# Kernel optimization log

Hardware: AMD Instinct MI355X
Metric: run time of the kernel (lower is better)

Reference implementation:

```python
import jax, jax.numpy as jnp
import numpy as np

EMB = 1024
HEADS = 16
EPS = 1e-6


def setup_inputs() -> dict:
    key = jax.random.key(0)
    ks = jax.random.split(key, 11)
    B, T = 4, 2048
    s = 0.02
    inp = {
        "x": jax.random.normal(ks[0], (B, T, EMB), dtype=jnp.float32),
        "Wq": jax.random.normal(ks[1], (EMB, EMB), dtype=jnp.float32) * s,
        "bq": jnp.zeros((EMB,), dtype=jnp.float32),
        "Wk": jax.random.normal(ks[2], (EMB, EMB), dtype=jnp.float32) * s,
        "bk": jnp.zeros((EMB,), dtype=jnp.float32),
        "Wv": jax.random.normal(ks[3], (EMB, EMB), dtype=jnp.float32) * s,
        "bv": jnp.zeros((EMB,), dtype=jnp.float32),
        "Wp": jax.random.normal(ks[4], (EMB, EMB), dtype=jnp.float32) * s,
        "bp": jnp.zeros((EMB,), dtype=jnp.float32),
        "gamma": jnp.ones((EMB,), dtype=jnp.float32),
        "beta": jnp.zeros((EMB,), dtype=jnp.float32),
    }
    return inp


def reference(x, Wq, bq, Wk, bk, Wv, bv, Wp, bp, gamma, beta):
    B, T, E = x.shape
    H = HEADS
    hd = E // H
    residual = x
    # torch Linear: y = x @ W.T + b
    q = (jnp.einsum('bte,fe->btf', x, Wq) + bq).reshape(B, T, H, hd).transpose(0, 2, 1, 3)
    k = (jnp.einsum('bte,fe->btf', x, Wk) + bk).reshape(B, T, H, hd).transpose(0, 2, 1, 3)
    v = (jnp.einsum('bte,fe->btf', x, Wv) + bv).reshape(B, T, H, hd).transpose(0, 2, 1, 3)
    # NOTE: original scales by 1/sqrt(T), not 1/sqrt(head_size)
    scale = 1.0 / jnp.sqrt(jnp.asarray(T, dtype=x.dtype))
    att = jnp.einsum('bhqd,bhkd->bhqk', q, k) * scale
    causal = jnp.tril(jnp.ones((T, T), dtype=bool))
    att = jnp.where(causal, att, -jnp.inf)
    att = jax.nn.softmax(att, axis=-1)
    out = jnp.einsum('bhqk,bhkd->bhqd', att, v)
    out = out.transpose(0, 2, 1, 3).reshape(B, T, E)
    # residual added BEFORE projection (as in original)
    out = jnp.einsum('bte,fe->btf', out + residual, Wp) + bp
    # LayerNorm(eps=1e-6)
    mu = jnp.mean(out, axis=-1, keepdims=True)
    var = jnp.mean(jnp.square(out - mu), axis=-1, keepdims=True)
    out = (out - mu) / jnp.sqrt(var + EPS) * gamma + beta
    return out
```

## Files before the change

### kernel.cpp

```cpp
#include <hip/hip_runtime.h>
#include <hip/hip_bf16.h>
#include <cstdint>
#include <cstdio>

#define EMB    1024
#define HEADS  16
#define HD     64
#define TSEQ   2048
#define NBATCH 4
#define BT     (NBATCH*TSEQ)
#define QKVN   3072
#define QKLD   2048

#define CSCALE (1.4426950408889634f * 0.022097086912079608f)

typedef __hip_bfloat16 bf16;
typedef __attribute__((ext_vector_type(8))) short short8;
typedef __attribute__((ext_vector_type(4))) short short4v;
typedef __attribute__((ext_vector_type(4))) float f32x4;

#define MFMA32(A,B,C) __builtin_amdgcn_mfma_f32_16x16x32_bf16(A,B,C,0,0,0)
#if __has_builtin(__builtin_amdgcn_mfma_f32_16x16x16_bf16)
#define MFMA16(A,B,C) __builtin_amdgcn_mfma_f32_16x16x16_bf16(A,B,C,0,0,0)
#else
#define MFMA16(A,B,C) __builtin_amdgcn_mfma_f32_16x16x16bf16_1k(A,B,C,0,0,0)
#endif

#if __has_builtin(__builtin_amdgcn_exp2f)
#define EXP2(x) __builtin_amdgcn_exp2f(x)
#else
#define EXP2(x) exp2f(x)
#endif

template<bool B> struct BoolC { static constexpr bool value = B; };

__device__ __forceinline__ void gload_lds16(const void* g, void* l) {
  __builtin_amdgcn_global_load_lds(
      (const __attribute__((address_space(1))) void*)g,
      (__attribute__((address_space(3))) void*)l,
      16, 0, 0);
}

__device__ __forceinline__ unsigned pkbf(float a, float b) {
  unsigned ua = __builtin_bit_cast(unsigned, a) + 0x8000u;
  unsigned ub = __builtin_bit_cast(unsigned, b) + 0x8000u;
  return __builtin_amdgcn_perm(ub, ua, 0x07060302u);
}

__global__ void fused_cast(const float* __restrict__ x, const float* __restrict__ Wq,
                           const float* __restrict__ Wk, const float* __restrict__ Wv,
                           const float* __restrict__ Wp, const float* __restrict__ bq,
                           const float* __restrict__ bk, const float* __restrict__ bv,
                           bf16* __restrict__ xb, bf16* __restrict__ wqkv,
                           bf16* __restrict__ wpb, float* __restrict__ biasqkv) {
  const int blk = blockIdx.x;
  const int i = threadIdx.x * 4;
  if (blk >= 12288) {
    const int wsel = blk - 12288;
    const float* bsrc = wsel == 0 ? bq : (wsel == 1 ? bk : bv);
    float4 bv4 = *(const float4*)(bsrc + i);
    if (wsel == 0) { bv4.x *= CSCALE; bv4.y *= CSCALE; bv4.z *= CSCALE; bv4.w *= CSCALE; }
    *(float4*)(biasqkv + wsel * 1024 + i) = bv4;
    return;
  }
  const float* src; bf16* dst; float sc = 1.0f;
  if (blk < 8192)       { src = x  + (size_t)blk * 1024;           dst = xb   + (size_t)blk * 1024; }
  else if (blk < 9216)  { src = Wq + (size_t)(blk - 8192) * 1024;  dst = wqkv + (size_t)(blk - 8192) * 1024; sc = CSCALE; }
  else if (blk < 10240) { src = Wk + (size_t)(blk - 9216) * 1024;  dst = wqkv + ((size_t)1 << 20) + (size_t)(blk - 9216) * 1024; }
  else if (blk < 11264) { src = Wv + (size_t)(blk - 10240) * 1024; dst = wqkv + ((size_t)2 << 20) + (size_t)(blk - 10240) * 1024; }
  else                  { src = Wp + (size_t)(blk - 11264) * 1024; dst = wpb  + (size_t)(blk - 11264) * 1024; }
  float4 v = *(const float4*)(src + i);
  union { short4v v; bf16 b[4]; } u;
  u.b[0] = __float2bfloat16(v.x * sc); u.b[1] = __float2bfloat16(v.y * sc);
  u.b[2] = __float2bfloat16(v.z * sc); u.b[3] = __float2bfloat16(v.w * sc);
  *(short4v*)(dst + i) = u.v;
}

template<int MODE>
__global__ __launch_bounds__(256) void gemm_bt(
    const bf16* __restrict__ A, const bf16* __restrict__ B,
    const float* __restrict__ bias, void* __restrict__ out0,
    bf16* __restrict__ vt, int M, int N, int K) {
  __shared__ bf16 As[128 * 32];
  __shared__ bf16 Bs[128 * 32];
  const int tid = threadIdx.x;
  const int l = tid & 63, w = tid >> 6;
  const int r = l & 15, q = l >> 4;
  const int m0 = blockIdx.y * 128, n0 = blockIdx.x * 128;
  const int wm = w >> 1, wn = w & 1;

  f32x4 acc[4][4];
#pragma unroll
  for (int i = 0; i < 4; ++i)
#pragma unroll
    for (int j = 0; j < 4; ++j) acc[i][j] = (f32x4){0.f, 0.f, 0.f, 0.f};

  const int slot0 = w * 64 + l;
  const int rowS0 = slot0 >> 2, chS0 = (slot0 & 3) * 8;
  const int slot1 = 256 + slot0;
  const int rowS1 = slot1 >> 2, chS1 = (slot1 & 3) * 8;

  const bf16* A0 = A + (size_t)(m0 + rowS0) * K + chS0;
  const bf16* A1 = A + (size_t)(m0 + rowS1) * K + chS1;
  const bf16* B0 = B + (size_t)(n0 + rowS0) * K + chS0;
  const bf16* B1 = B + (size_t)(n0 + rowS1) * K + chS1;
  char* AsD0 = (char*)As + w * 1024;
  char* AsD1 = (char*)As + 4096 + w * 1024;
  char* BsD0 = (char*)Bs + w * 1024;
  char* BsD1 = (char*)Bs + 4096 + w * 1024;

  for (int k0 = 0; k0 < K; k0 += 32) {
    __syncthreads();
    gload_lds16(A0 + k0, AsD0);
    gload_lds16(A1 + k0, AsD1);
    gload_lds16(B0 + k0, BsD0);
    gload_lds16(B1 + k0, BsD1);
    __syncthreads();

    short8 af[4], bfr[4];
#pragma unroll
    for (int mt = 0; mt < 4; ++mt)
      af[mt] = *(const short8*)(As + (wm * 64 + mt * 16 + r) * 32 + q * 8);
#pragma unroll
    for (int nt = 0; nt < 4; ++nt)
      bfr[nt] = *(const short8*)(Bs + (wn * 64 + nt * 16 + r) * 32 + q * 8);
#pragma unroll
    for (int mt = 0; mt < 4; ++mt)
#pragma unroll
      for (int nt = 0; nt < 4; ++nt)
        acc[mt][nt] = MFMA32(af[mt], bfr[nt], acc[mt][nt]);
  }

#pragma unroll
  for (int nt = 0; nt < 4; ++nt) {
    const int col = n0 + wn * 64 + nt * 16 + r;
    const float bv = bias[col];
#pragma unroll
    for (int mt = 0; mt < 4; ++mt) {
#pragma unroll
      for (int reg = 0; reg < 4; ++reg) {
        const int row = m0 + wm * 64 + mt * 16 + q * 4 + reg;
        const float v = acc[mt][nt][reg] + bv;
        if (MODE == 1) {
          ((float*)out0)[(size_t)row * N + col] = v;
        } else if (n0 < 2048) {
          ((bf16*)out0)[(size_t)row * QKLD + col] = __float2bfloat16(v);
        } else {
          const int f = col - 2048, h = f >> 6, d = f & 63;
          const int b = row >> 11, t = row & 2047;
          const int swz = (t & ~63) | ((((t >> 3) ^ d) & 7) << 3) | (t & 7);
          vt[((size_t)(b * 16 + h) * 64 + d) * 2048 + swz] = __float2bfloat16(v);
        }
      }
    }
  }
}

__global__ __launch_bounds__(256, 2) void flash5(
    const bf16* __restrict__ qk, const bf16* __restrict__ vt,
    const float* __restrict__ x, bf16* __restrict__ pb) {
  const int bh = blockIdx.x;
  const int ip = blockIdx.y;
  const int b = bh >> 4, h = bh & 15;
  const int qt[4] = { 31 - ip, 23 - ip, ip + 8, ip };
  const int tid = threadIdx.x, l = tid & 63, w = tid >> 6;
  const int r = l & 15, quad = l >> 4;

  __shared__ bf16 VtL[2][64 * 64];

  const bf16* Qbase = qk + (size_t)b * TSEQ * QKLD + h * HD;
  const bf16* Kbase = Qbase + 1024;
  const bf16* Vhead = vt + (size_t)bh * 64 * 2048;

  const int sl0 = tid, sl1 = 256 + tid;
  const bf16* vg0 = Vhead + (size_t)(sl0 >> 3) * 2048 + (sl0 & 7) * 8;
  const bf16* vg1 = Vhead + (size_t)(sl1 >> 3) * 2048 + (sl1 & 7) * 8;
  char* ldsb0[2] = { (char*)&VtL[0][0] + w * 1024, (char*)&VtL[1][0] + w * 1024 };
  char* ldsb1[2] = { (char*)&VtL[0][0] + 4096 + w * 1024, (char*)&VtL[1][0] + 4096 + w * 1024 };

  short8 qf0[4], qf1[4];
#pragma unroll
  for (int t = 0; t < 4; ++t) {
    const bf16* qp = Qbase + (size_t)(qt[t] * 64 + w * 16 + r) * QKLD + quad * 8;
    qf0[t] = *(const short8*)qp;
    qf1[t] = *(const short8*)(qp + 32);
  }

  f32x4 o[4][4], lac[4];
#pragma unroll
  for (int t = 0; t < 4; ++t) {
    lac[t] = (f32x4){0.f, 0.f, 0.f, 0.f};
#pragma unroll
    for (int nt = 0; nt < 4; ++nt) o[t][nt] = (f32x4){0.f, 0.f, 0.f, 0.f};
  }

  short4v ones4;
#pragma unroll
  for (int j = 0; j < 4; ++j) ones4[j] = (short)0x3F80;

  short8 kf0[4], kf1[4];
  short4v vf[4][4];

  gload_lds16(vg0, ldsb0[0]);
  gload_lds16(vg1, ldsb1[0]);
  int bsel = 0;

  const int ktmax = qt[0];
  const int qrow_l = w * 16 + r;
  for (int kt = 0; kt <= ktmax; ++kt) {
#pragma unroll
    for (int g = 0; g < 4; ++g) {
      const bf16* kp = Kbase + (size_t)(kt * 64 + g * 16 + r) * QKLD + quad * 8;
      kf0[g] = *(const short8*)kp;
      kf1[g] = *(const short8*)(kp + 32);
    }
    __syncthreads();
    if (kt < ktmax) {
      gload_lds16(vg0 + (kt + 1) * 64, ldsb0[bsel ^ 1]);
      gload_lds16(vg1 + (kt + 1) * 64, ldsb1[bsel ^ 1]);
    }
    {
      const bf16* V = &VtL[bsel][0];
#pragma unroll
      for (int nt = 0; nt < 4; ++nt)
#pragma unroll
        for (int g = 0; g < 4; ++g)
          vf[nt][g] = *(const short4v*)(V + (nt * 16 + r) * 64 +
                                        (((g * 2 + (quad >> 1)) ^ (r & 7)) * 8) + (quad & 1) * 4);
    }

    auto tilestep = [&](int t, auto diagc) {
      constexpr bool D = decltype(diagc)::value;
      f32x4 s[4];
#pragma unroll
      for (int g = 0; g < 4; ++g) {
        f32x4 a = (f32x4){0.f, 0.f, 0.f, 0.f};
        a = MFMA32(kf0[g], qf0[t], a);
        a = MFMA32(kf1[g], qf1[t], a);
        s[g] = a;
      }
      short4v pA[4];
#pragma unroll
      for (int g = 0; g < 4; ++g) {
        float p[4];
#pragma unroll
        for (int reg = 0; reg < 4; ++reg) {
          float e = EXP2(s[g][reg]);
          if (D) {
            const int kj = g * 16 + quad * 4 + reg;
            if (kj > qrow_l) e = 0.f;
          }
          p[reg] = e;
        }
        union { short4v v; unsigned u[2]; } pu;
        pu.u[0] = pkbf(p[0], p[1]);
        pu.u[1] = pkbf(p[2], p[3]);
        pA[g] = pu.v;
      }
#pragma unroll
      for (int nt = 0; nt < 4; ++nt)
#pragma unroll
        for (int g = 0; g < 4; ++g)
          o[t][nt] = MFMA16(pA[g], vf[nt][g], o[t][nt]);
#pragma unroll
      for (int g = 0; g < 4; ++g)
        lac[t] = MFMA16(pA[g], ones4, lac[t]);
    };

    if (kt == qt[0]) tilestep(0, BoolC<true>{}); else tilestep(0, BoolC<false>{});
    if (kt <= qt[1]) { if (kt == qt[1]) tilestep(1, BoolC<true>{}); else tilestep(1, BoolC<false>{}); }
    if (kt <= qt[2]) { if (kt == qt[2]) tilestep(2, BoolC<true>{}); else tilestep(2, BoolC<false>{}); }
    if (kt <= qt[3]) { if (kt == qt[3]) tilestep(3, BoolC<true>{}); else tilestep(3, BoolC<false>{}); }
    bsel ^= 1;
  }

#pragma unroll
  for (int t = 0; t < 4; ++t) {
#pragma unroll
    for (int reg = 0; reg < 4; ++reg) {
      const float inv = 1.0f / lac[t][reg];
      const int row = qt[t] * 64 + w * 16 + quad * 4 + reg;
      const float* xr = x + (size_t)(b * TSEQ + row) * EMB + h * HD;
      bf16* pr = pb + (size_t)(b * TSEQ + row) * EMB + h * HD;
#pragma unroll
      for (int nt = 0; nt < 4; ++nt) {
        const int d = nt * 16 + r;
        pr[d] = __float2bfloat16(o[t][nt][reg] * inv + xr[d]);
      }
    }
  }
}

__global__ __launch_bounds__(256) void ln_kernel(float* __restrict__ out,
                                                 const float* __restrict__ gamma,
                                                 const float* __restrict__ beta) {
  const int row = blockIdx.x;
  const int tid = threadIdx.x;
  float* p = out + (size_t)row * EMB;
  float4 v = ((const float4*)p)[tid];
  float s = v.x + v.y + v.z + v.w;
  float ss = v.x * v.x + v.y * v.y + v.z * v.z + v.w * v.w;
#pragma unroll
  for (int m = 1; m < 64; m <<= 1) {
    s += __shfl_xor(s, m, 64);
    ss += __shfl_xor(ss, m, 64);
  }
  __shared__ float red[8];
  const int w = tid >> 6, l = tid & 63;
  if (l == 0) { red[w] = s; red[4 + w] = ss; }
  __syncthreads();
  s = red[0] + red[1] + red[2] + red[3];
  ss = red[4] + red[5] + red[6] + red[7];
  const float mu = s * (1.0f / EMB);
  const float var = ss * (1.0f / EMB) - mu * mu;
  const float rs = rsqrtf(var + 1e-6f);
  const float4 g = ((const float4*)gamma)[tid];
  const float4 bb = ((const float4*)beta)[tid];
  float4 o;
  o.x = (v.x - mu) * rs * g.x + bb.x;
  o.y = (v.y - mu) * rs * g.y + bb.y;
  o.z = (v.z - mu) * rs * g.z + bb.z;
  o.w = (v.w - mu) * rs * g.w + bb.w;
  ((float4*)p)[tid] = o;
}

extern "C" void kernel_launch(void* const* d_in, const int* in_sizes, int n_in,
                              void* d_out, int out_size, void* d_ws, size_t ws_size,
                              hipStream_t stream) {
  const float* x     = (const float*)d_in[0];
  const float* Wq    = (const float*)d_in[1];
  const float* bq    = (const float*)d_in[2];
  const float* Wk    = (const float*)d_in[3];
  const float* bk    = (const float*)d_in[4];
  const float* Wv    = (const float*)d_in[5];
  const float* bv    = (const float*)d_in[6];
  const float* Wp    = (const float*)d_in[7];
  const float* bp    = (const float*)d_in[8];
  const float* gamma = (const float*)d_in[9];
  const float* beta  = (const float*)d_in[10];
  float* out = (float*)d_out;

  if (ws_size < (size_t)74 * 1024 * 1024) {
    printf("kernel_launch: ws_size %zu too small\n", ws_size);
    return;
  }
  char* ws = (char*)d_ws;
  bf16* xb    = (bf16*)ws;
  bf16* wqkv  = (bf16*)(ws + ((size_t)16 << 20));
  bf16* wpb   = (bf16*)(ws + ((size_t)22 << 20));
  float* bqkv = (float*)(ws + ((size_t)24 << 20));
  bf16* qkbuf = (bf16*)(ws + ((size_t)25 << 20));
  bf16* vtbuf = (bf16*)(ws + ((size_t)57 << 20));
  bf16* pbuf  = xb;

  fused_cast<<<12291, 256, 0, stream>>>(x, Wq, Wk, Wv, Wp, bq, bk, bv, xb, wqkv, wpb, bqkv);

  gemm_bt<0><<<dim3(24, 64), 256, 0, stream>>>(xb, wqkv, bqkv, qkbuf, vtbuf, BT, QKVN, EMB);

  flash5<<<dim3(64, 8), 256, 0, stream>>>(qkbuf, vtbuf, x, pbuf);

  gemm_bt<1><<<dim3(8, 64), 256, 0, stream>>>(pbuf, wpb, bp, out, nullptr, BT, EMB, EMB);

  ln_kernel<<<BT, 256, 0, stream>>>(out, gamma, beta);
}
```

Measured before the change: 311.7 us.

## Replace QKV GEMM with 256x256 double-buffered 8-wave pipelined kernel

Adds a new QKV projection GEMM that uses 256x256 output tiles, 512 threads, a 64-wide K step and double-buffered LDS. Global-to-LDS loads are interleaved with four MFMA phases per tile, using explicit barriers, vmcnt waits and s_setprio. It also applies an XOR-swizzled LDS layout and a grouped block-to-tile mapping aimed at L2 reuse. The goal is to hide memory latency and raise MFMA utilisation compared with the 128x128 generic kernel. In exchange it relies on hand-tuned wait counts, and the large accumulator arrays add register pressure.

```diff
diff --git a/kernel.cpp b/kernel.cpp
--- a/kernel.cpp
+++ b/kernel.cpp
@@ -46,6 +46,13 @@
   unsigned ub = __builtin_bit_cast(unsigned, b) + 0x8000u;
   return __builtin_amdgcn_perm(ub, ua, 0x07060302u);
 }
+
+#define BARRIER() do { asm volatile("" ::: "memory"); \
+                       __builtin_amdgcn_s_barrier(); \
+                       asm volatile("" ::: "memory"); } while (0)
+#define BAR_VM(N) do { asm volatile("s_waitcnt vmcnt(" #N ")" ::: "memory"); \
+                       __builtin_amdgcn_s_barrier(); \
+                       asm volatile("" ::: "memory"); } while (0)
 
 __global__ void fused_cast(const float* __restrict__ x, const float* __restrict__ Wq,
                            const float* __restrict__ Wk, const float* __restrict__ Wv,
@@ -74,6 +81,150 @@
   u.b[0] = __float2bfloat16(v.x * sc); u.b[1] = __float2bfloat16(v.y * sc);
   u.b[2] = __float2bfloat16(v.z * sc); u.b[3] = __float2bfloat16(v.w * sc);
   *(short4v*)(dst + i) = u.v;
+}
+
+#define PHASE_MFMA(MI0, NJ0) do { \
+  __builtin_amdgcn_s_setprio(1); \
+  _Pragma("unroll") \
+  for (int m2 = 0; m2 < 4; ++m2) { \
+    _Pragma("unroll") \
+    for (int n2 = 0; n2 < 2; ++n2) { \
+      acc[(MI0)+m2][(NJ0)+n2] = MFMA32(af[m2][0], bfr[(NJ0)+n2][0], acc[(MI0)+m2][(NJ0)+n2]); \
+      acc[(MI0)+m2][(NJ0)+n2] = MFMA32(af[m2][1], bfr[(NJ0)+n2][1], acc[(MI0)+m2][(NJ0)+n2]); \
+    } \
+  } \
+  __builtin_amdgcn_s_setprio(0); \
+} while (0)
+
+#define TILE(T, P) { \
+  const int kn = ((T) + 1) * 64; \
+  const bool st = (T) < 15; \
+  const char* aB = rdA + (P) * 32768; \
+  const char* bB = rdB + (P) * 32768; \
+  char* sA = ldsA + ((P) ^ 1) * 32768 + wbase; \
+  char* sB = ldsB + ((P) ^ 1) * 32768 + wbase; \
+   \
+  _Pragma("unroll") \
+  for (int m2 = 0; m2 < 4; ++m2) { \
+    af[m2][0] = *(const short8*)(aB + m2 * 2048 + cs0); \
+    af[m2][1] = *(const short8*)(aB + m2 * 2048 + cs1); \
+  } \
+  _Pragma("unroll") \
+  for (int n2 = 0; n2 < 2; ++n2) { \
+    bfr[n2][0] = *(const short8*)(bB + n2 * 2048 + cs0); \
+    bfr[n2][1] = *(const short8*)(bB + n2 * 2048 + cs1); \
+  } \
+  if (st) { gload_lds16(gB + kn,          sB);         \
+            gload_lds16(gB + 131072 + kn, sB + 16384); } \
+  BARRIER(); \
+  PHASE_MFMA(0, 0); \
+  BARRIER(); \
+   \
+  _Pragma("unroll") \
+  for (int n2 = 2; n2 < 4; ++n2) { \
+    bfr[n2][0] = *(const short8*)(bB + n2 * 2048 + cs0); \
+    bfr[n2][1] = *(const short8*)(bB + n2 * 2048 + cs1); \
+  } \
+  if (st) { gload_lds16(gA + kn,          sA);         \
+            gload_lds16(gA + 131072 + kn, sA + 16384); } \
+  BARRIER(); \
+  PHASE_MFMA(0, 2); \
+  if (st) { BAR_VM(4); } else { BAR_VM(0); } \
+   \
+  _Pragma("unroll") \
+  for (int m2 = 0; m2 < 4; ++m2) { \
+    af[m2][0] = *(const short8*)(aB + (4 + m2) * 2048 + cs0); \
+    af[m2][1] = *(const short8*)(aB + (4 + m2) * 2048 + cs1); \
+  } \
+  if (st) { gload_lds16(gB + 65536 + kn,  sB + 8192);  \
+            gload_lds16(gB + 196608 + kn, sB + 24576); } \
+  BARRIER(); \
+  PHASE_MFMA(4, 2); \
+  BARRIER(); \
+   \
+  if (st) { gload_lds16(gA + 65536 + kn,  sA + 8192);  \
+            gload_lds16(gA + 196608 + kn, sA + 24576); } \
+  PHASE_MFMA(4, 0); \
+  if (st) { BAR_VM(2); } \
+}
+
+__global__ __launch_bounds__(512, 2) void gemm_qkv8(
+    const bf16* __restrict__ A, const bf16* __restrict__ B,
+    const float* __restrict__ bias, bf16* __restrict__ qkout,
+    bf16* __restrict__ vt) {
+  __shared__ short smem[65536];
+  const int tid = threadIdx.x;
+  const int l = tid & 63, w = tid >> 6;
+  const int r = l & 15, qd = l >> 4;
+  const int wm = w >> 2, wn = w & 3;
+
+  const int f0 = blockIdx.x;
+  const int sid = (f0 & 7) * 48 + (f0 >> 3);
+  const int m0 = (sid / 12) * 256;
+  const int n0 = (sid % 12) * 256;
+
+  const int rowA = tid >> 3;
+  const int chk = (tid & 7) ^ (rowA & 7);
+  const bf16* gA = A + (size_t)(m0 + rowA) * 1024 + chk * 8;
+  const bf16* gB = B + (size_t)(n0 + rowA) * 1024 + chk * 8;
+  char* ldsA = (char*)smem;
+  char* ldsB = (char*)smem + 65536;
+  const int wbase = w * 1024;
+
+  const char* rdA = (const char*)smem + wm * 16384 + r * 128;
+  const char* rdB = (const char*)smem + 65536 + (wn >> 1) * 16384 +
+                    ((wn & 1) * 64 + r) * 128;
+  const int cs0 = (qd ^ (r & 7)) * 16;
+  const int cs1 = ((4 + qd) ^ (r & 7)) * 16;
+
+  f32x4 acc[8][4];
+#pragma unroll
+  for (int i = 0; i < 8; ++i)
+#pragma unroll
+    for (int j = 0; j < 4; ++j) acc[i][j] = (f32x4){0.f, 0.f, 0.f, 0.f};
+  short8 af[4][2], bfr[4][2];
+
+  {
+    char* sA = ldsA + wbase;
+    char* sB = ldsB + wbase;
+    gload_lds16(gB,          sB);
+    gload_lds16(gB + 131072, sB + 16384);
+    gload_lds16(gA,          sA);
+    gload_lds16(gA + 131072, sA + 16384);
+    gload_lds16(gB + 65536,  sB + 8192);
+    gload_lds16(gB + 196608, sB + 24576);
+    gload_lds16(gA + 65536,  sA + 8192);
+    gload_lds16(gA + 196608, sA + 24576);
+    BAR_VM(2);
+  }
+
+#pragma unroll 1
+  for (int tt = 0; tt < 8; ++tt) {
+    TILE(tt * 2, 0)
+    TILE(tt * 2 + 1, 1)
+  }
+
+#pragma unroll
+  for (int nt = 0; nt < 4; ++nt) {
+    const int col = n0 + wn * 64 + nt * 16 + r;
+    const float bv = bias[col];
+#pragma unroll
+    for (int mi = 0; mi < 8; ++mi) {
+#pragma unroll
+      for (int reg = 0; reg < 4; ++reg) {
+        const int row = m0 + wm * 128 + mi * 16 + qd * 4 + reg;
+        const float v = acc[mi][nt][reg] + bv;
+        if (n0 < 2048) {
+          qkout[(size_t)row * QKLD + col] = __float2bfloat16(v);
+        } else {
+          const int f = col - 2048, h = f >> 6, d = f & 63;
+          const int b = row >> 11, t = row & 2047;
+          const int swz = (t & ~63) | ((((t >> 3) ^ d) & 7) << 3) | (t & 7);
+          vt[((size_t)(b * 16 + h) * 64 + d) * 2048 + swz] = __float2bfloat16(v);
+        }
+      }
+    }
+  }
 }
 
 template<int MODE>
@@ -355,7 +506,7 @@
 
   fused_cast<<<12291, 256, 0, stream>>>(x, Wq, Wk, Wv, Wp, bq, bk, bv, xb, wqkv, wpb, bqkv);
 
-  gemm_bt<0><<<dim3(24, 64), 256, 0, stream>>>(xb, wqkv, bqkv, qkbuf, vtbuf, BT, QKVN, EMB);
+  gemm_qkv8<<<dim3(384), dim3(512), 0, stream>>>(xb, wqkv, bqkv, qkbuf, vtbuf);
 
   flash5<<<dim3(64, 8), 256, 0, stream>>>(qkbuf, vtbuf, x, pbuf);
 
```

Measured after the change: 306.6 us. No clear change (-1.6%).
